# Optimization experiments

Measured on AMD Instinct MI355X. Metric: run time of the kernel, lower is better.

Reference implementation:

```python
import jax, jax.numpy as jnp
import numpy as np

NEG_SLOPE = 0.01


def reference(feat_src, feat_dst, src, dst, attn_l, attn_r):
    # feat_src: [Ns, D], feat_dst: [Nd, D], src/dst: [E] int, attn_*: [1, D]
    n_dst = feat_dst.shape[0]
    el = (feat_src * attn_l).sum(axis=-1)  # [Ns]
    er = (feat_dst * attn_r).sum(axis=-1)  # [Nd]
    e = el[src] + er[dst]                  # [E]
    e = jnp.where(e >= 0, e, NEG_SLOPE * e)  # leaky_relu
    # edge softmax over incoming edges of each destination node
    m = jax.ops.segment_max(e, dst, num_segments=n_dst)  # [Nd]
    m = jnp.where(jnp.isfinite(m), m, 0.0)  # guard empty segments
    a = jnp.exp(e - m[dst])                 # [E]
    denom = jax.ops.segment_sum(a, dst, num_segments=n_dst)  # [Nd]
    denom = jnp.where(denom > 0, denom, 1.0)
    a = a / denom[dst]
    # weighted scatter-sum of source features: [E, D] messages -> [Nd, D]
    msg = feat_src[src] * a[:, None]
    out = jax.ops.segment_sum(msg, dst, num_segments=n_dst)
    return out


def setup_inputs() -> dict:
    key = jax.random.key(0)
    k1, k2, k3, k4, k5, k6 = jax.random.split(key, 6)
    Ns, Nd, E, D = 100000, 100000, 1600000, 128
    return {
        "feat_src": jax.random.normal(k1, (Ns, D), dtype=jnp.float32),
        "feat_dst": jax.random.normal(k2, (Nd, D), dtype=jnp.float32),
        "src": jax.random.randint(k3, (E,), 0, Ns, dtype=jnp.int32),
        "dst": jax.random.randint(k4, (E,), 0, Nd, dtype=jnp.int32),
        "attn_l": jax.random.normal(k5, (1, D), dtype=jnp.float32) * 0.1,
        "attn_r": jax.random.normal(k6, (1, D), dtype=jnp.float32) * 0.1,
    }
```

## Files before the change

### kernel.cpp

```cpp
#include <hip/hip_runtime.h>
#include <hip/hip_bf16.h>
#include <math.h>

#define D 128
#define AGG_THREADS 128
#define CHUNK 512
#define BSHIFT 8
#define MAXB 1024
#define MAXWG 1024
#define PCHUNK 4096
#define PE 16
#define EBUF_CAP 5120
#define PR 8192

__device__ __forceinline__ unsigned short f2bf(float f) {
    union { float f; unsigned int u; } c; c.f = f;
    unsigned int u = c.u;
    unsigned int r = (u + 0x7FFFu + ((u >> 16) & 1u)) >> 16;
    return (unsigned short)r;
}
__device__ __forceinline__ void unpack2(unsigned int w, float& lo, float& hi) {
    union { unsigned int u; float f; } c;
    c.u = w << 16;          lo = c.f;
    c.u = w & 0xFFFF0000u;  hi = c.f;
}

__global__ void prep_kernel(const float* __restrict__ feat_src,
                            const float* __restrict__ feat_dst,
                            const float* __restrict__ attn_l,
                            const float* __restrict__ attn_r,
                            float* __restrict__ el, float* __restrict__ er,
                            unsigned short* __restrict__ feat_bf, int store_bf,
                            int Ns, int Nd) {
    int half = threadIdx.x >> 5;
    int lane = threadIdx.x & 31;
    int node = blockIdx.x * 8 + half;
    if (node >= Ns + Nd) return;
    bool is_src = node < Ns;
    const float* feat = is_src ? feat_src + (size_t)node * D
                               : feat_dst + (size_t)(node - Ns) * D;
    const float* attn = is_src ? attn_l : attn_r;
    float4 a = ((const float4*)attn)[lane];
    float4 v = ((const float4*)feat)[lane];
    if (is_src && store_bf) {
        ushort4 h; h.x = f2bf(v.x); h.y = f2bf(v.y); h.z = f2bf(v.z); h.w = f2bf(v.w);
        ((ushort4*)(feat_bf + (size_t)node * D))[lane] = h;
    }
    float s = v.x * a.x + v.y * a.y + v.z * a.z + v.w * a.w;
    #pragma unroll
    for (int off = 16; off > 0; off >>= 1)
        s += __shfl_xor(s, off, 64);
    if (lane == 0) {
        if (is_src) el[node] = s;
        else        er[node - Ns] = s;
    }
}

__global__ void partition_kernel(const int* __restrict__ src, const int* __restrict__ dst,
                                 int E, int nbk,
                                 uint2* __restrict__ bins,
                                 int* __restrict__ cnt_tab, int* __restrict__ loc_tab) {
    __shared__ int hist[MAXB];
    __shared__ int lstart[MAXB];
    __shared__ int cursor[MAXB];
    __shared__ uint2 sbuf[PCHUNK];
    int w = blockIdx.x, tid = threadIdx.x;
    int e0 = w * PCHUNK;
    int e1 = min(E, e0 + PCHUNK);
    int n = e1 - e0;

    for (int i = tid; i < nbk; i += 256) hist[i] = 0;
    __syncthreads();

    int es[PE], ed[PE];
    #pragma unroll
    for (int k = 0; k < PE; ++k) {
        int idx = e0 + k * 256 + tid;
        if (idx < e1) {
            es[k] = src[idx];
            ed[k] = dst[idx];
            atomicAdd(&hist[ed[k] >> BSHIFT], 1);
        }
    }
    __syncthreads();

    if (tid < 64) {
        int carry = 0;
        for (int c = 0; c < nbk; c += 64) {
            int i = c + tid;
            int v = (i < nbk) ? hist[i] : 0;
            int x = v;
            #pragma unroll
            for (int off = 1; off < 64; off <<= 1) {
                int t = __shfl_up(x, off, 64);
                if (tid >= off) x += t;
            }
            if (i < nbk) lstart[i] = x - v + carry;
            carry += __shfl(x, 63, 64);
        }
    }
    __syncthreads();

    for (int i = tid; i < nbk; i += 256) {
        cnt_tab[(size_t)w * nbk + i] = hist[i];
        loc_tab[(size_t)w * nbk + i] = lstart[i];
        cursor[i] = 0;
    }
    __syncthreads();

    #pragma unroll
    for (int k = 0; k < PE; ++k) {
        int idx = e0 + k * 256 + tid;
        if (idx < e1) {
            int b = ed[k] >> BSHIFT;
            int r = lstart[b] + atomicAdd(&cursor[b], 1);
            sbuf[r] = make_uint2((unsigned)es[k], (unsigned)ed[k]);
        }
    }
    __syncthreads();

    uint2* obase = bins + (size_t)w * PCHUNK;
    for (int t = tid; t < n; t += 256) obase[t] = sbuf[t];
}

__global__ void bucket_kernel(const uint2* __restrict__ bins,
                              const int* __restrict__ cnt_tab, const int* __restrict__ loc_tab,
                              int nbk, int nwg,
                              int* __restrict__ counts, int* __restrict__ offs,
                              int* __restrict__ perm, int Nd) {
    __shared__ uint2 ebuf[EBUF_CAP];
    __shared__ int wcnt[MAXWG];
    __shared__ int wdst[MAXWG];
    __shared__ int cnt256[256];
    __shared__ int off256[256];
    __shared__ int cur256[256];
    __shared__ int tile[256];
    __shared__ int total_sh;

    int b = blockIdx.x, tid = threadIdx.x;
    int base = b << BSHIFT;

    for (int i = tid; i < nwg; i += 256) wcnt[i] = cnt_tab[(size_t)i * nbk + b];
    __syncthreads();
    if (tid < 64) {
        int carry = 0;
        for (int c = 0; c < nwg; c += 64) {
            int i = c + tid;
            int v = (i < nwg) ? wcnt[i] : 0;
            int x = v;
            #pragma unroll
            for (int off = 1; off < 64; off <<= 1) {
                int t = __shfl_up(x, off, 64);
                if (tid >= off) x += t;
            }
            if (i < nwg) wdst[i] = x - v + carry;
            carry += __shfl(x, 63, 64);
        }
        if (tid == 0) total_sh = carry;
    }
    cnt256[tid] = 0;
    cur256[tid] = 0;
    __syncthreads();
    int n = total_sh;
    bool fits = (n <= EBUF_CAP);

    if (fits) {
        for (int w = tid; w < nwg; w += 256) {
            int c = wcnt[w];
            if (c) {
                const uint2* sp = bins + (size_t)w * PCHUNK + loc_tab[(size_t)w * nbk + b];
                int d0 = wdst[w];
                for (int k = 0; k < c; ++k) ebuf[d0 + k] = sp[k];
            }
        }
        __syncthreads();
        for (int t = tid; t < n; t += 256)
            atomicAdd(&cnt256[(int)ebuf[t].y - base], 1);
    } else {
        for (int w = tid; w < nwg; w += 256) {
            int c = wcnt[w];
            const uint2* sp = bins + (size_t)w * PCHUNK + loc_tab[(size_t)w * nbk + b];
            for (int k = 0; k < c; ++k)
                atomicAdd(&cnt256[(int)sp[k].y - base], 1);
        }
        __syncthreads();
    }
    __syncthreads();

    int v = cnt256[tid];
    tile[tid] = v;
    __syncthreads();
    for (int off = 1; off < 256; off <<= 1) {
        int t = (tid >= off) ? tile[tid - off] : 0;
        __syncthreads();
        tile[tid] += t;
        __syncthreads();
    }
    int myoff = tile[tid] - v;
    off256[tid] = myoff;
    int i = base + tid;
    if (i < Nd) {
        int c = v;
        if (myoff + c > PR) c = max(0, PR - myoff);
        counts[i] = c;
        offs[i]   = myoff;
    }
    __syncthreads();

    size_t rbase = (size_t)b * PR;
    if (fits) {
        for (int t = tid; t < n; t += 256) {
            uint2 e = ebuf[t];
            int d = (int)e.y - base;
            int r = atomicAdd(&cur256[d], 1);
            int slot = off256[d] + r;
            if (slot < PR) perm[rbase + slot] = (int)e.x;
        }
    } else {
        for (int w = tid; w < nwg; w += 256) {
            int c = wcnt[w];
            const uint2* sp = bins + (size_t)w * PCHUNK + loc_tab[(size_t)w * nbk + b];
            for (int k = 0; k < c; ++k) {
                uint2 e = sp[k];
                int d = (int)e.y - base;
                int r = atomicAdd(&cur256[d], 1);
                int slot = off256[d] + r;
                if (slot < PR) perm[rbase + slot] = (int)e.x;
            }
        }
    }
}

__device__ __forceinline__ float block_max128(float v, float* red, int tid) {
    #pragma unroll
    for (int off = 32; off > 0; off >>= 1)
        v = fmaxf(v, __shfl_down(v, off, 64));
    __syncthreads();
    if ((tid & 63) == 0) red[tid >> 6] = v;
    __syncthreads();
    return fmaxf(red[0], red[1]);
}
__device__ __forceinline__ float block_sum128(float v, float* red, int tid) {
    #pragma unroll
    for (int off = 32; off > 0; off >>= 1)
        v += __shfl_down(v, off, 64);
    __syncthreads();
    if ((tid & 63) == 0) red[tid >> 6] = v;
    __syncthreads();
    return red[0] + red[1];
}

__global__ void gat_aggregate_bf16_kernel(const unsigned short* __restrict__ feat_bf,
                                          const float* __restrict__ el,
                                          const float* __restrict__ er,
                                          const int* __restrict__ offs,
                                          const int* __restrict__ counts,
                                          const int* __restrict__ perm,
                                          float* __restrict__ out, int Nd) {
    __shared__ float w_sh[CHUNK];
    __shared__ int   s_sh[CHUNK];
    __shared__ float red[2];
    __shared__ float acc_sh[8][D];

    int j = blockIdx.x;
    int tid = threadIdx.x;
    int cnt = counts[j];
    size_t orow = (size_t)j * D;
    if (cnt == 0) { out[orow + tid] = 0.0f; return; }

    size_t beg = (size_t)(j >> BSHIFT) * PR + offs[j];
    float erj = er[j];
    int g = tid >> 4, u = tid & 15;
    float acc[8];
    #pragma unroll
    for (int k = 0; k < 8; ++k) acc[k] = 0.0f;
    float inv;
    const unsigned short* fb = feat_bf + (size_t)u * 8;

    if (cnt <= CHUNK) {
        float lmax = -INFINITY;
        for (int t = tid; t < cnt; t += AGG_THREADS) {
            int s = perm[beg + t];
            float e = el[s] + erj;
            e = (e >= 0.0f) ? e : 0.01f * e;
            s_sh[t] = s;
            w_sh[t] = e;
            lmax = fmaxf(lmax, e);
        }
        float m = block_max128(lmax, red, tid);
        float lsum = 0.0f;
        for (int t = tid; t < cnt; t += AGG_THREADS) {
            float a = __expf(w_sh[t] - m);
            w_sh[t] = a;
            lsum += a;
        }
        float den = block_sum128(lsum, red, tid);
        inv = 1.0f / den;
        __syncthreads();
        for (int t = g; t < cnt; t += 8) {
            int s = s_sh[t];
            float w = w_sh[t];
            uint4 v = *(const uint4*)(fb + (size_t)s * D);
            float f[8];
            unpack2(v.x, f[0], f[1]); unpack2(v.y, f[2], f[3]);
            unpack2(v.z, f[4], f[5]); unpack2(v.w, f[6], f[7]);
            #pragma unroll
            for (int k = 0; k < 8; ++k) acc[k] += w * f[k];
        }
    } else {
        float lmax = -INFINITY;
        for (int t = tid; t < cnt; t += AGG_THREADS) {
            int s = perm[beg + t];
            float e = el[s] + erj;
            e = (e >= 0.0f) ? e : 0.01f * e;
            lmax = fmaxf(lmax, e);
        }
        float m = block_max128(lmax, red, tid);
        float lsum = 0.0f;
        for (int t = tid; t < cnt; t += AGG_THREADS) {
            int s = perm[beg + t];
            float e = el[s] + erj;
            e = (e >= 0.0f) ? e : 0.01f * e;
            lsum += __expf(e - m);
        }
        float den = block_sum128(lsum, red, tid);
        inv = 1.0f / den;
        for (int bb = 0; bb < cnt; bb += CHUNK) {
            int n = min(CHUNK, cnt - bb);
            __syncthreads();
            for (int t = tid; t < n; t += AGG_THREADS) {
                int s = perm[beg + bb + t];
                float e = el[s] + erj;
                e = (e >= 0.0f) ? e : 0.01f * e;
                s_sh[t] = s;
                w_sh[t] = __expf(e - m);
            }
            __syncthreads();
            for (int t = g; t < n; t += 8) {
                int s = s_sh[t];
                float w = w_sh[t];
                uint4 v = *(const uint4*)(fb + (size_t)s * D);
                float f[8];
                unpack2(v.x, f[0], f[1]); unpack2(v.y, f[2], f[3]);
                unpack2(v.z, f[4], f[5]); unpack2(v.w, f[6], f[7]);
                #pragma unroll
                for (int k = 0; k < 8; ++k) acc[k] += w * f[k];
            }
        }
    }
    #pragma unroll
    for (int k = 0; k < 8; ++k) acc_sh[g][u * 8 + k] = acc[k];
    __syncthreads();
    float r = 0.0f;
    #pragma unroll
    for (int g2 = 0; g2 < 8; ++g2) r += acc_sh[g2][tid];
    out[orow + tid] = r * inv;
}

__global__ void hist_kernel(const int* __restrict__ dst, int E, int* __restrict__ counts) {
    int stride = gridDim.x * blockDim.x;
    for (int k = blockIdx.x * blockDim.x + threadIdx.x; k < E; k += stride)
        atomicAdd(&counts[dst[k]], 1);
}
__global__ void scan1_kernel(const int* __restrict__ counts, int* __restrict__ offsets,
                             int* __restrict__ blockSums, int N) {
    __shared__ int tile[256];
    int tid = threadIdx.x;
    int i = blockIdx.x * 256 + tid;
    int v = (i < N) ? counts[i] : 0;
    tile[tid] = v;
    __syncthreads();
    for (int off = 1; off < 256; off <<= 1) {
        int t = (tid >= off) ? tile[tid - off] : 0;
        __syncthreads();
        tile[tid] += t;
        __syncthreads();
    }
    int incl = tile[tid];
    if (i < N) offsets[i] = incl - v;
    if (tid == 255) blockSums[blockIdx.x] = incl;
}
__global__ void scan2_kernel(int* __restrict__ bs, int nb) {
    __shared__ int tile[256];
    int tid = threadIdx.x;
    int carry = 0;
    for (int base = 0; base < nb; base += 256) {
        int i = base + tid;
        int v = (i < nb) ? bs[i] : 0;
        __syncthreads();
        tile[tid] = v;
        __syncthreads();
        for (int off = 1; off < 256; off <<= 1) {
            int t = (tid >= off) ? tile[tid - off] : 0;
            __syncthreads();
            tile[tid] += t;
            __syncthreads();
        }
        int incl = tile[tid];
        if (i < nb) bs[i] = incl - v + carry;
        carry += tile[255];
    }
}
__global__ void fill_kernel(const int* __restrict__ src, const int* __restrict__ dst, int E,
                            const int* __restrict__ offsets, const int* __restrict__ bsum,
                            int* __restrict__ cursor, int* __restrict__ perm_src) {
    int stride = gridDim.x * blockDim.x;
    for (int k = blockIdx.x * blockDim.x + threadIdx.x; k < E; k += stride) {
        int j = dst[k];
        int p = offsets[j] + bsum[j >> BSHIFT] + atomicAdd(&cursor[j], 1);
        perm_src[p] = src[k];
    }
}
__global__ void gat_aggregate_f32_kernel(const float* __restrict__ feat_src,
                                         const float* __restrict__ el,
                                         const float* __restrict__ er,
                                         const int* __restrict__ offsets,
                                         const int* __restrict__ bsum,
                                         const int* __restrict__ counts,
                                         const int* __restrict__ perm_src,
                                         float* __restrict__ out, int Nd) {
    __shared__ float w_sh[CHUNK];
    __shared__ int   s_sh[CHUNK];
    __shared__ float red[2];
    int j = blockIdx.x;
    int tid = threadIdx.x;
    int cnt = counts[j];
    size_t orow = (size_t)j * D;
    if (cnt == 0) { out[orow + tid] = 0.0f; return; }
    int beg = offsets[j] + bsum[j >> BSHIFT];
    float erj = er[j];
    float acc = 0.0f;
    float inv;
    if (cnt <= CHUNK) {
        float lmax = -INFINITY;
        for (int t = tid; t < cnt; t += AGG_THREADS) {
            int s = perm_src[beg + t];
            float e = el[s] + erj;
            e = (e >= 0.0f) ? e : 0.01f * e;
            s_sh[t] = s; w_sh[t] = e;
            lmax = fmaxf(lmax, e);
        }
        float m = block_max128(lmax, red, tid);
        float lsum = 0.0f;
        for (int t = tid; t < cnt; t += AGG_THREADS) {
            float a = __expf(w_sh[t] - m);
            w_sh[t] = a; lsum += a;
        }
        float den = block_sum128(lsum, red, tid);
        inv = 1.0f / den;
        __syncthreads();
        for (int t = 0; t < cnt; ++t)
            acc += feat_src[(size_t)s_sh[t] * D + tid] * w_sh[t];
    } else {
        float lmax = -INFINITY;
        for (int t = tid; t < cnt; t += AGG_THREADS) {
            int s = perm_src[beg + t];
            float e = el[s] + erj;
            e = (e >= 0.0f) ? e : 0.01f * e;
            lmax = fmaxf(lmax, e);
        }
        float m = block_max128(lmax, red, tid);
        float lsum = 0.0f;
        for (int t = tid; t < cnt; t += AGG_THREADS) {
            int s = perm_src[beg + t];
            float e = el[s] + erj;
            e = (e >= 0.0f) ? e : 0.01f * e;
            lsum += __expf(e - m);
        }
        float den = block_sum128(lsum, red, tid);
        inv = 1.0f / den;
        for (int bb = 0; bb < cnt; bb += CHUNK) {
            int n = min(CHUNK, cnt - bb);
            __syncthreads();
            for (int t = tid; t < n; t += AGG_THREADS) {
                int s = perm_src[beg + bb + t];
                float e = el[s] + erj;
                e = (e >= 0.0f) ? e : 0.01f * e;
                s_sh[t] = s;
                w_sh[t] = __expf(e - m);
            }
            __syncthreads();
            for (int t = 0; t < n; ++t)
                acc += feat_src[(size_t)s_sh[t] * D + tid] * w_sh[t];
        }
    }
    out[orow + tid] = acc * inv;
}

extern "C" void kernel_launch(void* const* d_in, const int* in_sizes, int n_in,
                              void* d_out, int out_size, void* d_ws, size_t ws_size,
                              hipStream_t stream) {
    const float* feat_src = (const float*)d_in[0];
    const float* feat_dst = (const float*)d_in[1];
    const int*   src      = (const int*)d_in[2];
    const int*   dst      = (const int*)d_in[3];
    const float* attn_l   = (const float*)d_in[4];
    const float* attn_r   = (const float*)d_in[5];
    float* out = (float*)d_out;

    int Ns = in_sizes[0] / D;
    int Nd = in_sizes[1] / D;
    int E  = in_sizes[2];
    int NBK = (Nd + (1 << BSHIFT) - 1) >> BSHIFT;
    int NWG = (E + PCHUNK - 1) / PCHUNK;

    char* p = (char*)d_ws;
    auto carve = [&](size_t bytes) { void* r = (void*)p; p += (bytes + 255) & ~(size_t)255; return r; };
    float* el      = (float*)carve((size_t)Ns * 4);
    float* er      = (float*)carve((size_t)Nd * 4);
    int*   counts  = (int*)carve((size_t)Nd * 4);
    int*   offs    = (int*)carve((size_t)Nd * 4);
    int*   gcursor = (int*)carve((size_t)Nd * 4);
    int*   bsums   = (int*)carve((size_t)NBK * 4);
    int*   cnt_tab = (int*)carve((size_t)NWG * NBK * 4);
    int*   loc_tab = (int*)carve((size_t)NWG * NBK * 4);
    int*   perm    = (int*)carve((size_t)NBK * PR * 4);
    uint2* bins    = (uint2*)carve((size_t)NWG * PCHUNK * 8);
    size_t used    = (size_t)(p - (char*)d_ws);
    size_t bf_bytes = (size_t)Ns * D * 2;
    unsigned short* feat_bf = (unsigned short*)carve(bf_bytes);

    int fast = (NBK <= MAXB && NWG <= MAXWG &&
                used + bf_bytes + 256 <= ws_size) ? 1 : 0;

    int total = Ns + Nd;
    if (fast) {
        prep_kernel<<<(total + 7) / 8, 256, 0, stream>>>(feat_src, feat_dst, attn_l, attn_r,
                                                         el, er, feat_bf, 1, Ns, Nd);
        partition_kernel<<<NWG, 256, 0, stream>>>(src, dst, E, NBK, bins, cnt_tab, loc_tab);
        bucket_kernel<<<NBK, 256, 0, stream>>>(bins, cnt_tab, loc_tab, NBK, NWG,
                                               counts, offs, perm, Nd);
        gat_aggregate_bf16_kernel<<<Nd, AGG_THREADS, 0, stream>>>(feat_bf, el, er, offs,
                                                                  counts, perm, out, Nd);
    } else {
        hipMemsetAsync(counts, 0, (size_t)Nd * 4, stream);
        hipMemsetAsync(gcursor, 0, (size_t)Nd * 4, stream);
        prep_kernel<<<(total + 7) / 8, 256, 0, stream>>>(feat_src, feat_dst, attn_l, attn_r,
                                                         el, er, nullptr, 0, Ns, Nd);
        hist_kernel<<<2048, 256, 0, stream>>>(dst, E, counts);
        scan1_kernel<<<NBK, 256, 0, stream>>>(counts, offs, bsums, Nd);
        scan2_kernel<<<1, 256, 0, stream>>>(bsums, NBK);
        fill_kernel<<<2048, 256, 0, stream>>>(src, dst, E, offs, bsums, gcursor, perm);
        gat_aggregate_f32_kernel<<<Nd, AGG_THREADS, 0, stream>>>(feat_src, el, er, offs,
                                                                 bsums, counts, perm, out, Nd);
    }
}
```

Measured before the change: 277.6 us.

## Aggregate one destination per wavefront and parallelize bucket gather

The aggregation kernel now assigns one 64-lane wavefront per destination node, four nodes per 256-thread block. Softmax reductions use wave shuffles instead of shared memory and block barriers, and edge indices and weights are broadcast by shuffle rather than staged in LDS. The bucket kernel's per-workgroup serial copy loop is replaced by a per-edge binary search over the workgroup prefix offsets, which spreads the gather evenly across threads. In exchange it adds a log(nwg) search per edge, and nodes with more than 64 edges now recompute edge scores across three passes.

```diff
diff --git a/kernel.cpp b/kernel.cpp
--- a/kernel.cpp
+++ b/kernel.cpp
@@ -131,6 +131,7 @@
     __shared__ uint2 ebuf[EBUF_CAP];
     __shared__ int wcnt[MAXWG];
     __shared__ int wdst[MAXWG];
+    __shared__ int sbase[MAXWG];
     __shared__ int cnt256[256];
     __shared__ int off256[256];
     __shared__ int cur256[256];
@@ -165,17 +166,19 @@
     bool fits = (n <= EBUF_CAP);
 
     if (fits) {
-        for (int w = tid; w < nwg; w += 256) {
-            int c = wcnt[w];
-            if (c) {
-                const uint2* sp = bins + (size_t)w * PCHUNK + loc_tab[(size_t)w * nbk + b];
-                int d0 = wdst[w];
-                for (int k = 0; k < c; ++k) ebuf[d0 + k] = sp[k];
-            }
-        }
-        __syncthreads();
-        for (int t = tid; t < n; t += 256)
-            atomicAdd(&cnt256[(int)ebuf[t].y - base], 1);
+        for (int w = tid; w < nwg; w += 256)
+            sbase[w] = w * PCHUNK + loc_tab[(size_t)w * nbk + b] - wdst[w];
+        __syncthreads();
+        for (int t = tid; t < n; t += 256) {
+            int lo = 0, hi = nwg - 1;
+            while (lo < hi) {
+                int mid = (lo + hi + 1) >> 1;
+                if (wdst[mid] <= t) lo = mid; else hi = mid - 1;
+            }
+            uint2 e = bins[(size_t)(sbase[lo] + t)];
+            ebuf[t] = e;
+            atomicAdd(&cnt256[(int)e.y - base], 1);
+        }
     } else {
         for (int w = tid; w < nwg; w += 256) {
             int c = wcnt[w];
@@ -250,96 +253,56 @@
     return red[0] + red[1];
 }
 
-__global__ void gat_aggregate_bf16_kernel(const unsigned short* __restrict__ feat_bf,
+__global__ void gat_aggregate_wave_kernel(const unsigned short* __restrict__ feat_bf,
                                           const float* __restrict__ el,
                                           const float* __restrict__ er,
                                           const int* __restrict__ offs,
                                           const int* __restrict__ counts,
                                           const int* __restrict__ perm,
                                           float* __restrict__ out, int Nd) {
-    __shared__ float w_sh[CHUNK];
-    __shared__ int   s_sh[CHUNK];
-    __shared__ float red[2];
-    __shared__ float acc_sh[8][D];
-
-    int j = blockIdx.x;
-    int tid = threadIdx.x;
+    int wid  = threadIdx.x >> 6;
+    int lane = threadIdx.x & 63;
+    int j = blockIdx.x * 4 + wid;
+    if (j >= Nd) return;
     int cnt = counts[j];
     size_t orow = (size_t)j * D;
-    if (cnt == 0) { out[orow + tid] = 0.0f; return; }
-
-    size_t beg = (size_t)(j >> BSHIFT) * PR + offs[j];
+    if (cnt == 0) {
+        ((float2*)(out + orow))[lane] = make_float2(0.0f, 0.0f);
+        return;
+    }
+    size_t beg = (size_t)(j >> BSHIFT) * PR + (size_t)offs[j];
     float erj = er[j];
-    int g = tid >> 4, u = tid & 15;
+    int sg = lane >> 4, u = lane & 15;
+    const unsigned short* fb = feat_bf + (size_t)u * 8;
     float acc[8];
     #pragma unroll
     for (int k = 0; k < 8; ++k) acc[k] = 0.0f;
-    float inv;
-    const unsigned short* fb = feat_bf + (size_t)u * 8;
-
-    if (cnt <= CHUNK) {
-        float lmax = -INFINITY;
-        for (int t = tid; t < cnt; t += AGG_THREADS) {
-            int s = perm[beg + t];
-            float e = el[s] + erj;
-            e = (e >= 0.0f) ? e : 0.01f * e;
-            s_sh[t] = s;
-            w_sh[t] = e;
-            lmax = fmaxf(lmax, e);
-        }
-        float m = block_max128(lmax, red, tid);
-        float lsum = 0.0f;
-        for (int t = tid; t < cnt; t += AGG_THREADS) {
-            float a = __expf(w_sh[t] - m);
-            w_sh[t] = a;
-            lsum += a;
-        }
-        float den = block_sum128(lsum, red, tid);
-        inv = 1.0f / den;
-        __syncthreads();
-        for (int t = g; t < cnt; t += 8) {
-            int s = s_sh[t];
-            float w = w_sh[t];
-            uint4 v = *(const uint4*)(fb + (size_t)s * D);
-            float f[8];
-            unpack2(v.x, f[0], f[1]); unpack2(v.y, f[2], f[3]);
-            unpack2(v.z, f[4], f[5]); unpack2(v.w, f[6], f[7]);
-            #pragma unroll
-            for (int k = 0; k < 8; ++k) acc[k] += w * f[k];
-        }
-    } else {
-        float lmax = -INFINITY;
-        for (int t = tid; t < cnt; t += AGG_THREADS) {
-            int s = perm[beg + t];
-            float e = el[s] + erj;
-            e = (e >= 0.0f) ? e : 0.01f * e;
-            lmax = fmaxf(lmax, e);
-        }
-        float m = block_max128(lmax, red, tid);
-        float lsum = 0.0f;
-        for (int t = tid; t < cnt; t += AGG_THREADS) {
-            int s = perm[beg + t];
-            float e = el[s] + erj;
-            e = (e >= 0.0f) ? e : 0.01f * e;
-            lsum += __expf(e - m);
-        }
-        float den = block_sum128(lsum, red, tid);
-        inv = 1.0f / den;
-        for (int bb = 0; bb < cnt; bb += CHUNK) {
-            int n = min(CHUNK, cnt - bb);
-            __syncthreads();
-            for (int t = tid; t < n; t += AGG_THREADS) {
-                int s = perm[beg + bb + t];
-                float e = el[s] + erj;
-                e = (e >= 0.0f) ? e : 0.01f * e;
-                s_sh[t] = s;
-                w_sh[t] = __expf(e - m);
-            }
-            __syncthreads();
-            for (int t = g; t < n; t += 8) {
-                int s = s_sh[t];
-                float w = w_sh[t];
-                uint4 v = *(const uint4*)(fb + (size_t)s * D);
+
+    if (cnt <= 64) {
+        int s = 0; float e = -INFINITY;
+        if (lane < cnt) {
+            s = perm[beg + lane];
+            float t = el[s] + erj;
+            e = (t >= 0.0f) ? t : 0.01f * t;
+        }
+        float m = e;
+        #pragma unroll
+        for (int off = 32; off > 0; off >>= 1)
+            m = fmaxf(m, __shfl_xor(m, off, 64));
+        float a = (lane < cnt) ? __expf(e - m) : 0.0f;
+        float den = a;
+        #pragma unroll
+        for (int off = 32; off > 0; off >>= 1)
+            den += __shfl_xor(den, off, 64);
+        a *= (1.0f / den);
+        int nit = (cnt + 3) >> 2;
+        for (int it = 0; it < nit; ++it) {
+            int t = sg + (it << 2);
+            int tt = (t < cnt) ? t : 0;
+            float w = __shfl(a, tt, 64);
+            int st  = __shfl(s, tt, 64);
+            if (t < cnt) {
+                uint4 v = *(const uint4*)(fb + (size_t)st * D);
                 float f[8];
                 unpack2(v.x, f[0], f[1]); unpack2(v.y, f[2], f[3]);
                 unpack2(v.z, f[4], f[5]); unpack2(v.w, f[6], f[7]);
@@ -347,14 +310,65 @@
                 for (int k = 0; k < 8; ++k) acc[k] += w * f[k];
             }
         }
-    }
-    #pragma unroll
-    for (int k = 0; k < 8; ++k) acc_sh[g][u * 8 + k] = acc[k];
-    __syncthreads();
-    float r = 0.0f;
-    #pragma unroll
-    for (int g2 = 0; g2 < 8; ++g2) r += acc_sh[g2][tid];
-    out[orow + tid] = r * inv;
+    } else {
+        float lmax = -INFINITY;
+        for (int t = lane; t < cnt; t += 64) {
+            int s = perm[beg + t];
+            float e = el[s] + erj;
+            e = (e >= 0.0f) ? e : 0.01f * e;
+            lmax = fmaxf(lmax, e);
+        }
+        float m = lmax;
+        #pragma unroll
+        for (int off = 32; off > 0; off >>= 1)
+            m = fmaxf(m, __shfl_xor(m, off, 64));
+        float lsum = 0.0f;
+        for (int t = lane; t < cnt; t += 64) {
+            int s = perm[beg + t];
+            float e = el[s] + erj;
+            e = (e >= 0.0f) ? e : 0.01f * e;
+            lsum += __expf(e - m);
+        }
+        #pragma unroll
+        for (int off = 32; off > 0; off >>= 1)
+            lsum += __shfl_xor(lsum, off, 64);
+        float inv = 1.0f / lsum;
+        for (int bb = 0; bb < cnt; bb += 64) {
+            int nn = min(64, cnt - bb);
+            int s = 0; float a = 0.0f;
+            if (lane < nn) {
+                s = perm[beg + bb + lane];
+                float e = el[s] + erj;
+                e = (e >= 0.0f) ? e : 0.01f * e;
+                a = __expf(e - m) * inv;
+            }
+            int nit = (nn + 3) >> 2;
+            for (int it = 0; it < nit; ++it) {
+                int t = sg + (it << 2);
+                int tt = (t < nn) ? t : 0;
+                float w = __shfl(a, tt, 64);
+                int st  = __shfl(s, tt, 64);
+                if (t < nn) {
+                    uint4 v = *(const uint4*)(fb + (size_t)st * D);
+                    float f[8];
+                    unpack2(v.x, f[0], f[1]); unpack2(v.y, f[2], f[3]);
+                    unpack2(v.z, f[4], f[5]); unpack2(v.w, f[6], f[7]);
+                    #pragma unroll
+                    for (int k = 0; k < 8; ++k) acc[k] += w * f[k];
+                }
+            }
+        }
+    }
+    #pragma unroll
+    for (int k = 0; k < 8; ++k) {
+        acc[k] += __shfl_xor(acc[k], 16, 64);
+        acc[k] += __shfl_xor(acc[k], 32, 64);
+    }
+    if (sg == 0) {
+        float* op = out + orow + (size_t)u * 8;
+        ((float4*)op)[0] = make_float4(acc[0], acc[1], acc[2], acc[3]);
+        ((float4*)op)[1] = make_float4(acc[4], acc[5], acc[6], acc[7]);
+    }
 }
 
 __global__ void hist_kernel(const int* __restrict__ dst, int E, int* __restrict__ counts) {
@@ -530,8 +544,8 @@
         partition_kernel<<<NWG, 256, 0, stream>>>(src, dst, E, NBK, bins, cnt_tab, loc_tab);
         bucket_kernel<<<NBK, 256, 0, stream>>>(bins, cnt_tab, loc_tab, NBK, NWG,
                                                counts, offs, perm, Nd);
-        gat_aggregate_bf16_kernel<<<Nd, AGG_THREADS, 0, stream>>>(feat_bf, el, er, offs,
-                                                                  counts, perm, out, Nd);
+        gat_aggregate_wave_kernel<<<(Nd + 3) / 4, 256, 0, stream>>>(feat_bf, el, er, offs,
+                                                                    counts, perm, out, Nd);
     } else {
         hipMemsetAsync(counts, 0, (size_t)Nd * 4, stream);
         hipMemsetAsync(gcursor, 0, (size_t)Nd * 4, stream);
```

Result: faster. 265.1 us (-4.5%).
